# Kernel optimization log

Measured on AMD Instinct MI355X. Metric: run time of the kernel, lower is better.

Reference implementation:

```python
import jax, jax.numpy as jnp
import numpy as np

B, N = 8, 1024          # batch_size, num_tracks
NKNN = 4                # n nearest neighbours
OUT_DIM = 32
EMB = OUT_DIM // NKNN   # per-neighbour embedding dim = 8
IN_DIM = 4              # rel position (2) + rel velocity (2)


def setup_inputs() -> dict:
    key = jax.random.key(0)
    k1, k2, k3, k4 = jax.random.split(key, 4)
    obs1 = jax.random.normal(k1, (B, N, 2), jnp.float32)
    obs2 = jax.random.normal(k2, (B, N, 2), jnp.float32)
    # Linear(IN_DIM, EMB) params
    W = jax.random.normal(k3, (EMB, IN_DIM), jnp.float32) * 0.1
    b = jax.random.normal(k4, (EMB,), jnp.float32) * 0.01
    return {"obs1": obs1, "obs2": obs2, "W": W, "b": b}


def _off_diag_idx(n):
    # idx[i, k] = k-th column index of row i skipping the diagonal (order preserved)
    idx = jnp.arange(n - 1)[None, :]
    return idx + (idx >= jnp.arange(n)[:, None])  # [n, n-1] int32


def reference(obs1, obs2, W, b):
    n = obs2.shape[1]
    # pairwise relative position / velocity: [B, N, N, 2]
    rel_pos = obs2[:, None, :, :] - obs2[:, :, None, :]
    vel = obs2 - obs1
    rel_dir = vel[:, None, :, :] - vel[:, :, None, :]

    # delete diagonal -> [B, N, N-1, 2]
    gidx = _off_diag_idx(n)[None, :, :, None]
    rel_pos = jnp.take_along_axis(rel_pos, gidx, axis=2)
    rel_dir = jnp.take_along_axis(rel_dir, gidx, axis=2)

    overall_grid = jnp.concatenate([rel_pos, rel_dir], axis=-1)  # [B,N,N-1,4]

    rel_distance = jnp.linalg.norm(rel_pos, axis=-1)             # [B,N,N-1]
    rel_distance = jnp.nan_to_num(rel_distance, nan=1000.0)

    # top-n nearest (smallest distance) -> gather their features
    _, dist_index = jax.lax.top_k(-rel_distance, NKNN)           # [B,N,n]
    nearest_grid = jnp.take_along_axis(
        overall_grid, dist_index[..., None], axis=2)             # [B,N,n,4]
    nearest_grid = jnp.nan_to_num(nearest_grid)

    # tiny Linear + ReLU embedding
    emb = jax.nn.relu(jnp.einsum('bnkf,ef->bnke', nearest_grid, W) + b)
    return emb.reshape(obs2.shape[0] * n, -1)                    # [B*N, 32]
```

## Files before the change

kernel.cpp:

```cpp
#include <hip/hip_runtime.h>
#include <math.h>

#define BATCH 8
#define NTR   1024

__global__ __launch_bounds__(256)
void knn_mm3(const float* __restrict__ obs1,
             const float* __restrict__ obs2,
             const float* __restrict__ W,
             const float* __restrict__ bias,
             float* __restrict__ out)
{
    __shared__ __align__(16) float2 sh_pos[NTR];
    __shared__ __align__(16) float4 sh_v[256];
    __shared__ int sh_idx[4][4];

    const int tid   = threadIdx.x;
    const int lane  = tid & 63;
    const int wv    = tid >> 6;
    const int batch = blockIdx.x >> 8;
    const int i     = ((blockIdx.x & 255) << 2) + wv;

    const float4* __restrict__ p2 = (const float4*)(obs2 + (size_t)batch * NTR * 2);
    float4* sp4 = (float4*)sh_pos;
    sp4[tid]       = p2[tid];
    sp4[tid + 256] = p2[tid + 256];
    __syncthreads();

    const float2 my = sh_pos[i];

    float s0 = 3e38f, s1 = 3e38f, s2 = 3e38f, s3 = 3e38f;
    float dd[16];

#pragma unroll
    for (int c = 0; c < 16; ++c) {
        const int j = lane + (c << 6);
        const float2 pj = sh_pos[j];
        const float dx = pj.x - my.x;
        const float dy = pj.y - my.y;
        float d = __fadd_rn(__fmul_rn(dx, dx), __fmul_rn(dy, dy));
        d = (j == i) ? 3e38f : d;
        dd[c] = d;
        const float t0 = fminf(s0, d);
        const float t1 = __builtin_amdgcn_fmed3f(s0, s1, d);
        const float t2 = __builtin_amdgcn_fmed3f(s1, s2, d);
        const float t3 = __builtin_amdgcn_fmed3f(s2, s3, d);
        s0 = t0; s1 = t1; s2 = t2; s3 = t3;
    }

    sh_v[tid] = make_float4(s0, s1, s2, s3);
    for (int half = 32; half >= 1; half >>= 1) {
        __syncthreads();
        if (lane < half) {
            const float4 o = sh_v[tid + half];
            float m0 = fminf(s0, o.w);
            float m1 = fminf(s1, o.z);
            float m2 = fminf(s2, o.y);
            float m3 = fminf(s3, o.x);
            float a, b;
            a = fminf(m0, m2); b = fmaxf(m0, m2); m0 = a; m2 = b;
            a = fminf(m1, m3); b = fmaxf(m1, m3); m1 = a; m3 = b;
            a = fminf(m0, m1); b = fmaxf(m0, m1); m0 = a; m1 = b;
            a = fminf(m2, m3); b = fmaxf(m2, m3); m2 = a; m3 = b;
            s0 = m0; s1 = m1; s2 = m2; s3 = m3;
            sh_v[tid] = make_float4(s0, s1, s2, s3);
        }
    }
    __syncthreads();

    const float4 v = sh_v[wv << 6];

#pragma unroll
    for (int c = 0; c < 16; ++c) {
        if (dd[c] <= v.w) {
            const int j = lane + (c << 6);
            const int rank = (int)(dd[c] > v.x) + (int)(dd[c] > v.y)
                           + (int)(dd[c] > v.z);
            sh_idx[wv][rank] = j;
        }
    }
    __syncthreads();

    if (tid < 128) {
        const int rr  = tid >> 5;
        const int kk  = (tid >> 3) & 3;
        const int e   = tid & 7;
        const int row = ((blockIdx.x & 255) << 2) + rr;

        int j = sh_idx[rr][kk] & (NTR - 1);

        const float2 pj  = sh_pos[j];
        const float2 myr = sh_pos[row];
        const float2* __restrict__ o1 = (const float2*)(obs1 + (size_t)batch * NTR * 2);
        const float2 o1j = o1[j];
        const float2 o1r = o1[row];
        const float f0 = pj.x - myr.x;
        const float f1 = pj.y - myr.y;
        const float f2 = (pj.x - o1j.x) - (myr.x - o1r.x);
        const float f3 = (pj.y - o1j.y) - (myr.y - o1r.y);

        const float4 w = ((const float4*)W)[e];
        float r = f0 * w.x + f1 * w.y + f2 * w.z + f3 * w.w + bias[e];
        r = fmaxf(r, 0.0f);

        out[(((size_t)(batch * NTR + ((blockIdx.x & 255) << 2))) << 5) + tid] = r;
    }
}

extern "C" void kernel_launch(void* const* d_in, const int* in_sizes, int n_in,
                              void* d_out, int out_size, void* d_ws, size_t ws_size,
                              hipStream_t stream) {
    const float* obs1 = (const float*)d_in[0];
    const float* obs2 = (const float*)d_in[1];
    const float* W    = (const float*)d_in[2];
    const float* bias = (const float*)d_in[3];
    float* out = (float*)d_out;

    const int grid = BATCH * (NTR / 4);
    knn_mm3<<<grid, 256, 0, stream>>>(obs1, obs2, W, bias, out);
}
```

Before: 11.98 us.

## Use float4 LDS loads for candidates and drop block barriers in wave-local reduction

Each lane now reads two candidate positions with one float4 LDS load, and the j index mapping and self-exclusion test are changed to match. The per-wave top-4 tree reduction drops its __syncthreads calls and keeps only compiler memory fences, relying on all 64 lanes of a wave executing in lockstep. The goal is fewer LDS instructions and no block-wide barriers. The risk is that without a barrier or wave-level fence the LDS ordering between lanes is not guaranteed, and the final read of sh_v and the writes to sh_idx may race.

```diff
diff --git a/kernel.cpp b/kernel.cpp
--- a/kernel.cpp
+++ b/kernel.cpp
@@ -5,11 +5,11 @@
 #define NTR   1024
 
 __global__ __launch_bounds__(256)
-void knn_mm3(const float* __restrict__ obs1,
-             const float* __restrict__ obs2,
-             const float* __restrict__ W,
-             const float* __restrict__ bias,
-             float* __restrict__ out)
+void knn_v9(const float* __restrict__ obs1,
+            const float* __restrict__ obs2,
+            const float* __restrict__ W,
+            const float* __restrict__ bias,
+            float* __restrict__ out)
 {
     __shared__ __align__(16) float2 sh_pos[NTR];
     __shared__ __align__(16) float4 sh_v[256];
@@ -29,53 +29,74 @@
 
     const float2 my = sh_pos[i];
 
+    const int  c_self    = i >> 7;
+    const bool self_even = (lane == ((i >> 1) & 63)) && ((i & 1) == 0);
+    const bool self_odd  = (lane == ((i >> 1) & 63)) && ((i & 1) == 1);
+
     float s0 = 3e38f, s1 = 3e38f, s2 = 3e38f, s3 = 3e38f;
     float dd[16];
 
+    const float4* pos4 = (const float4*)sh_pos;
 #pragma unroll
-    for (int c = 0; c < 16; ++c) {
-        const int j = lane + (c << 6);
-        const float2 pj = sh_pos[j];
-        const float dx = pj.x - my.x;
-        const float dy = pj.y - my.y;
-        float d = __fadd_rn(__fmul_rn(dx, dx), __fmul_rn(dy, dy));
-        d = (j == i) ? 3e38f : d;
-        dd[c] = d;
-        const float t0 = fminf(s0, d);
-        const float t1 = __builtin_amdgcn_fmed3f(s0, s1, d);
-        const float t2 = __builtin_amdgcn_fmed3f(s1, s2, d);
-        const float t3 = __builtin_amdgcn_fmed3f(s2, s3, d);
-        s0 = t0; s1 = t1; s2 = t2; s3 = t3;
+    for (int c = 0; c < 8; ++c) {
+        const float4 pq = pos4[(c << 6) + lane];
+        const float dx0 = pq.x - my.x;
+        const float dy0 = pq.y - my.y;
+        const float dx1 = pq.z - my.x;
+        const float dy1 = pq.w - my.y;
+        float d0 = __fadd_rn(__fmul_rn(dx0, dx0), __fmul_rn(dy0, dy0));
+        float d1 = __fadd_rn(__fmul_rn(dx1, dx1), __fmul_rn(dy1, dy1));
+        if (c == c_self) {
+            d0 = self_even ? 3e38f : d0;
+            d1 = self_odd  ? 3e38f : d1;
+        }
+        dd[2 * c]     = d0;
+        dd[2 * c + 1] = d1;
+        {
+            const float t0 = fminf(s0, d0);
+            const float t1 = __builtin_amdgcn_fmed3f(s0, s1, d0);
+            const float t2 = __builtin_amdgcn_fmed3f(s1, s2, d0);
+            const float t3 = __builtin_amdgcn_fmed3f(s2, s3, d0);
+            s0 = t0; s1 = t1; s2 = t2; s3 = t3;
+        }
+        {
+            const float t0 = fminf(s0, d1);
+            const float t1 = __builtin_amdgcn_fmed3f(s0, s1, d1);
+            const float t2 = __builtin_amdgcn_fmed3f(s1, s2, d1);
+            const float t3 = __builtin_amdgcn_fmed3f(s2, s3, d1);
+            s0 = t0; s1 = t1; s2 = t2; s3 = t3;
+        }
     }
 
     sh_v[tid] = make_float4(s0, s1, s2, s3);
+    asm volatile("" ::: "memory");
+#pragma unroll
     for (int half = 32; half >= 1; half >>= 1) {
-        __syncthreads();
         if (lane < half) {
             const float4 o = sh_v[tid + half];
             float m0 = fminf(s0, o.w);
             float m1 = fminf(s1, o.z);
             float m2 = fminf(s2, o.y);
             float m3 = fminf(s3, o.x);
-            float a, b;
-            a = fminf(m0, m2); b = fmaxf(m0, m2); m0 = a; m2 = b;
-            a = fminf(m1, m3); b = fmaxf(m1, m3); m1 = a; m3 = b;
-            a = fminf(m0, m1); b = fmaxf(m0, m1); m0 = a; m1 = b;
-            a = fminf(m2, m3); b = fmaxf(m2, m3); m2 = a; m3 = b;
+            float a;
+            a = fminf(m0, m2); m2 = fmaxf(m0, m2); m0 = a;
+            a = fminf(m1, m3); m3 = fmaxf(m1, m3); m1 = a;
+            a = fminf(m0, m1); m1 = fmaxf(m0, m1); m0 = a;
+            a = fminf(m2, m3); m3 = fmaxf(m2, m3); m2 = a;
             s0 = m0; s1 = m1; s2 = m2; s3 = m3;
             sh_v[tid] = make_float4(s0, s1, s2, s3);
         }
+        asm volatile("" ::: "memory");
     }
-    __syncthreads();
 
     const float4 v = sh_v[wv << 6];
 
 #pragma unroll
-    for (int c = 0; c < 16; ++c) {
-        if (dd[c] <= v.w) {
-            const int j = lane + (c << 6);
-            const int rank = (int)(dd[c] > v.x) + (int)(dd[c] > v.y)
-                           + (int)(dd[c] > v.z);
+    for (int k = 0; k < 16; ++k) {
+        if (dd[k] <= v.w) {
+            const int j = ((k >> 1) << 7) + (lane << 1) + (k & 1);
+            const int rank = (int)(dd[k] > v.x) + (int)(dd[k] > v.y)
+                           + (int)(dd[k] > v.z);
             sh_idx[wv][rank] = j;
         }
     }
@@ -117,5 +138,5 @@
     float* out = (float*)d_out;
 
     const int grid = BATCH * (NTR / 4);
-    knn_mm3<<<grid, 256, 0, stream>>>(obs1, obs2, W, bias, out);
+    knn_v9<<<grid, 256, 0, stream>>>(obs1, obs2, W, bias, out);
 }
```

Measured after the change: 11.79 us. Within noise of the previous version (-1.6%).
